# Optimization experiments

Measured on AMD Instinct MI355X. Metric: run time of the kernel, lower is better.

## Reference

```python
import jax, jax.numpy as jnp
import numpy as np

N_Q = 8        # qubits
DENC = 3       # encoding entangling layers
DVAR = 3       # variational entangling layers
SEQ = 64
BATCH = 256
D_FEAT = N_Q * (DENC + 2)   # 40, per-token feature dim
D_W = N_Q * (DVAR + 2)      # 40, per-position weight dim


def _rx(t):
    c = jnp.cos(t / 2).astype(jnp.complex64)
    s = (-1j * jnp.sin(t / 2)).astype(jnp.complex64)
    return jnp.stack([jnp.stack([c, s]), jnp.stack([s, c])])


def _ry(t):
    c = jnp.cos(t / 2)
    s = jnp.sin(t / 2)
    return jnp.stack([jnp.stack([c, -s]), jnp.stack([s, c])]).astype(jnp.complex64)


def _apply1(state, U, wire):
    # state: (2,)*N_Q complex; apply 2x2 gate on `wire`
    s = jnp.tensordot(U, state, axes=([1], [wire]))
    return jnp.moveaxis(s, 0, wire)


def _cnot(state, c, t):
    s0 = jnp.take(state, 0, axis=c)
    s1 = jnpp_flip = jnp.take(state, 1, axis=c)
    t2 = t - 1 if t > c else t
    s1 = jnp.flip(s1, axis=t2)  # X on target when control=1
    return jnp.stack([s0, s1], axis=c)


def _circuit(x, w, sign):
    # x: [D_FEAT] encoding angles, w: [D_W] variational angles
    state = jnp.zeros((2,) * N_Q, jnp.complex64).at[(0,) * N_Q].set(1.0)
    idx = 0
    for j in range(N_Q):
        state = _apply1(state, _rx(x[idx]), j)
        state = _apply1(state, _ry(x[idx + 1]), j)
        idx += 2
    for _ in range(DENC):
        for j in range(N_Q):
            state = _cnot(state, j, (j + 1) % N_Q)
        for j in range(N_Q):
            state = _apply1(state, _ry(x[idx]), j)
            idx += 1
    idx = 0
    for j in range(N_Q):
        state = _apply1(state, _rx(w[idx]), j)
        state = _apply1(state, _ry(w[idx + 1]), j)
        idx += 2
    for _ in range(DVAR):
        for j in range(N_Q):
            state = _cnot(state, j, (j + 1) % N_Q)
        for j in range(N_Q):
            state = _apply1(state, _ry(w[idx]), j)
            idx += 1
    probs = (jnp.abs(state) ** 2).astype(jnp.float32)
    return jnp.sum(probs * sign)


# observable sign tables
_Z0 = jnp.array([1.0, -1.0], jnp.float32).reshape((2,) + (1,) * (N_Q - 1))
_ZALL = jnp.array([1.0, -1.0], jnp.float32)
for _ in range(N_Q - 1):
    _ZALL = _ZALL[..., None] * jnp.array([1.0, -1.0], jnp.float32)


def _batched(sign):
    f = lambda xx, ww: _circuit(xx, ww, sign)
    f = jax.vmap(f, in_axes=(0, 0))      # over seq positions (per-position weights)
    return jax.vmap(f, in_axes=(0, None))  # over batch


_qk = _batched(_Z0)
_v = _batched(_ZALL)  # random_op fixed deterministically to Z x Z x ... x Z


def setup_inputs() -> dict:
    key = jax.random.key(0)
    k1, k2, k3, k4 = jax.random.split(key, 4)
    scale = np.float32(np.pi / 4)
    x = jax.random.normal(k1, (BATCH, SEQ, D_FEAT), jnp.float32)
    pQ = scale * (2 * jax.random.normal(k2, (SEQ, D_W), jnp.float32) - 1)
    pK = scale * (2 * jax.random.normal(k3, (SEQ, D_W), jnp.float32) - 1)
    pV = scale * (2 * jax.random.normal(k4, (SEQ, D_W), jnp.float32) - 1)
    return {"x": x, "params_Q": pQ, "params_K": pK, "params_V": pV}


def reference(x, params_Q, params_K, params_V):
    # Per-token quantum circuit sims -> scalar Q, K, V expectations
    Q = _qk(x, params_Q)   # [B, S]
    K = _qk(x, params_K)   # [B, S]
    V = _v(x, params_V)    # [B, S]  (original returns d identical copies of this)
    # Gaussian-kernel attention: alpha[b,i,m] = exp(-(Q_i - K_m)^2)
    alpha = jnp.exp(-(Q[:, :, None] - K[:, None, :]) ** 2)   # [B, S, S]
    w = alpha / jnp.sum(alpha, axis=-1, keepdims=True)
    att = jnp.einsum('bim,bm->bi', w, V)                     # [B, S]
    return x + att[:, :, None]  # broadcast over d (V copies are identical)
```

## Files before the change

### kernel.cpp

```cpp
#include <hip/hip_runtime.h>

#define SEQd 64
#define BATCHd 256
#define DF 40

typedef float f2 __attribute__((ext_vector_type(2)));
typedef __fp16 h2v __attribute__((ext_vector_type(2)));


template<int LM>
__device__ __forceinline__ float xch1(float v) {
  if constexpr (LM == 0) {
    return v;
  } else if constexpr (LM == 1 || LM == 2 || LM == 3 || LM == 7) {
    constexpr int ctrl = (LM == 1) ? 0xB1 : (LM == 2) ? 0x4E : (LM == 3) ? 0x1B
                       : 0x141;
    return __int_as_float(__builtin_amdgcn_mov_dpp(__float_as_int(v), ctrl, 0xF, 0xF, true));
  } else {
    return __int_as_float(__builtin_amdgcn_ds_swizzle(__float_as_int(v), (LM << 10) | 0x1F));
  }
}

template<int LM>
__device__ __forceinline__ f2 xch2(f2 v) {
  if constexpr (LM == 0) return v;
  f2 r; r.x = xch1<LM>(v.x); r.y = xch1<LM>(v.y); return r;
}

__device__ __forceinline__ f2 ff(f2 x, f2 y, f2 z) { return __builtin_elementwise_fma(x, y, z); }
__device__ __forceinline__ f2 cmul(f2 a, f2 b) {
  f2 r; r.x = a.x * b.x - a.y * b.y; r.y = a.x * b.y + a.y * b.x; return r;
}
__device__ __forceinline__ f2 uget(float4 f, bool bit) {
  f2 r; r.x = bit ? f.z : f.x; r.y = bit ? -f.w : f.y; return r;
}

template<int M, int SM>
__device__ __forceinline__ void ry32(f2* a, f2 cs, int lam) {
  constexpr int LM = M & 7, RM = M >> 3, SL = SM & 7, SR = SM >> 3;
  float t0;
  if constexpr (SL != 0) t0 = (__popc(lam & SL) & 1) ? cs.y : -cs.y;
  else                   t0 = -cs.y;
  const f2 cv = {cs.x, cs.x};
  const f2 tp = {t0, t0}, tn = {-t0, -t0};
#pragma unroll
  for (int k = 0; k < 32; ++k) {
    const int kp = k ^ RM;
    if (kp < k) continue;
    if (kp == k) {
      const f2 b = xch2<LM>(a[k]);
      a[k] = ff(b, (__builtin_popcount(k & SR) & 1) ? tn : tp, a[k] * cv);
    } else {
      const f2 b0 = xch2<LM>(a[kp]);
      const f2 b1 = xch2<LM>(a[k]);
      const f2 t_k  = (__builtin_popcount(k  & SR) & 1) ? tn : tp;
      const f2 t_kp = (__builtin_popcount(kp & SR) & 1) ? tn : tp;
      a[k]  = ff(b0, t_k,  a[k]  * cv);
      a[kp] = ff(b1, t_kp, a[kp] * cv);
    }
  }
}

template<int M, int SM>
__device__ __forceinline__ void su2_32(f2* a, float4 q, int lam) {
  constexpr int LM = M & 7, RM = M >> 3, SL = SM & 7, SR = SM >> 3;
  float sb, sc;
  if constexpr (SL != 0) {
    const bool p = (__popc(lam & SL) & 1) != 0;
    sb = p ? -q.y : q.y; sc = p ? -q.z : q.z;
  } else { sb = q.y; sc = q.z; }
  const f2 vqa = {q.x, q.x};
  const f2 vqw = {q.w, -q.w};
  const f2 vfc0 = {-sc, -sc}, vfb0 = {-sb, sb};
  const f2 vfc1 = { sc,  sc}, vfb1 = { sb, -sb};
#pragma unroll
  for (int k = 0; k < 32; ++k) {
    const int kp = k ^ RM;
    if (kp < k) continue;
    if (kp == k) {
      const f2 B = xch2<LM>(a[k]);
      const bool pk = (__builtin_popcount(k & SR) & 1) != 0;
      const f2 A = a[k];
      f2 r = A * vqa;
      r = ff(B, pk ? vfc1 : vfc0, r);
      r = ff(A.yx, pk ? vfb1 : vfb0, r);
      r = ff(B.yx, vqw, r);
      a[k] = r;
    } else {
      const f2 B0 = xch2<LM>(a[kp]);
      const f2 B1 = xch2<LM>(a[k]);
      const bool pk0 = (__builtin_popcount(k  & SR) & 1) != 0;
      const bool pk1 = (__builtin_popcount(kp & SR) & 1) != 0;
      const f2 A0 = a[k], A1 = a[kp];
      f2 r0 = A0 * vqa;
      r0 = ff(B0, pk0 ? vfc1 : vfc0, r0);
      r0 = ff(A0.yx, pk0 ? vfb1 : vfb0, r0);
      r0 = ff(B0.yx, vqw, r0);
      a[k] = r0;
      f2 r1 = A1 * vqa;
      r1 = ff(B1, pk1 ? vfc1 : vfc0, r1);
      r1 = ff(A1.yx, pk1 ? vfb1 : vfb0, r1);
      r1 = ff(B1.yx, vqw, r1);
      a[kp] = r1;
    }
  }
}

__device__ __forceinline__ void layers32(f2* a, const f2* __restrict__ L, int lam) {
  ry32<0xC0,0x7F>(a, L[0],  lam);
  ry32<0x60,0xC0>(a, L[1],  lam);
  ry32<0x30,0xE0>(a, L[2],  lam);
  ry32<0x18,0xF0>(a, L[3],  lam);
  ry32<0x0C,0xF8>(a, L[4],  lam);
  ry32<0x06,0xFC>(a, L[5],  lam);
  ry32<0x03,0xFE>(a, L[6],  lam);
  ry32<0xC1,0xFF>(a, L[7],  lam);
  ry32<0xA0,0xD5>(a, L[8],  lam);
  ry32<0x50,0xBF>(a, L[9],  lam);
  ry32<0x28,0x5F>(a, L[10], lam);
  ry32<0x14,0xAF>(a, L[11], lam);
  ry32<0x0A,0x57>(a, L[12], lam);
  ry32<0x05,0xAB>(a, L[13], lam);
  ry32<0xC2,0x55>(a, L[14], lam);
  ry32<0x61,0xAA>(a, L[15], lam);
  ry32<0xF0,0x4C>(a, L[16], lam);
  ry32<0x78,0x6A>(a, L[17], lam);
  ry32<0x3C,0x35>(a, L[18], lam);
  ry32<0x1E,0x9A>(a, L[19], lam);
  ry32<0x0F,0xCD>(a, L[20], lam);
  ry32<0xC7,0x66>(a, L[21], lam);
  ry32<0xA3,0x33>(a, L[22], lam);
  ry32<0x91,0x99>(a, L[23], lam);
}

__device__ __forceinline__ void initial32(f2* a, const float4* __restrict__ F, int lam) {
  su2_32<0x80,0x80>(a, F[0], lam);
  su2_32<0x40,0x40>(a, F[1], lam);
  su2_32<0x20,0x20>(a, F[2], lam);
  su2_32<0x10,0x10>(a, F[3], lam);
  su2_32<0x08,0x08>(a, F[4], lam);
  su2_32<0x04,0x04>(a, F[5], lam);
  su2_32<0x02,0x02>(a, F[6], lam);
  su2_32<0x01,0x01>(a, F[7], lam);
}

__device__ __forceinline__ void pinit32(f2* a, const float4* __restrict__ F, int lam) {
  f2 c = {1.f, 0.f};
#pragma unroll
  for (int i = 0; i < 3; ++i)
    c = cmul(c, uget(F[7 - i], ((lam >> i) & 1) != 0));
  f2 wlo[4], whi[8];
#pragma unroll
  for (int t = 0; t < 4; ++t)
    wlo[t] = cmul(uget(F[4], (t & 1) != 0), uget(F[3], ((t >> 1) & 1) != 0));
#pragma unroll
  for (int t = 0; t < 8; ++t)
    whi[t] = cmul(cmul(uget(F[2], (t & 1) != 0), uget(F[1], ((t >> 1) & 1) != 0)),
                  uget(F[0], ((t >> 2) & 1) != 0));
#pragma unroll
  for (int k = 0; k < 32; ++k)
    a[k] = cmul(cmul(c, wlo[k & 3]), whi[k >> 2]);
}

__device__ __forceinline__ uint32_t packh(f2 v) {
  h2v h = __builtin_amdgcn_cvt_pkrtz(v.x, v.y);
  return __builtin_bit_cast(uint32_t, h);
}
__device__ __forceinline__ f2 unpackh(uint32_t u) {
  h2v h = __builtin_bit_cast(h2v, u);
  f2 r; r.x = (float)h[0]; r.y = (float)h[1]; return r;
}

__device__ __forceinline__ void snap_write32(const f2* a, uint32_t* sn, int lam) {
  int tgt = 0;
  if (lam & 1) tgt ^= 0x2B;
  if (lam & 2) tgt ^= 0x56;
  if (lam & 4) tgt ^= 0xAC;
#pragma unroll
  for (int k = 0; k < 32; ++k) {
    const int rck = ((k & 1) ? 0xD9 : 0) ^ ((k & 2) ? 0x33 : 0) ^ ((k & 4) ? 0x66 : 0)
                  ^ ((k & 8) ? 0xCC : 0) ^ ((k & 16) ? 0x19 : 0);
    const int qq = tgt ^ rck;
    sn[(qq & 7) * 36 + (qq >> 3)] = packh(a[k]);
  }
}

__device__ __forceinline__ void snap_read32(f2* a, const uint32_t* sn, int lam) {
  const uint4* p = (const uint4*)(sn + lam * 36);
#pragma unroll
  for (int t = 0; t < 8; ++t) {
    const uint4 w = p[t];
    a[4*t+0] = unpackh(w.x); a[4*t+1] = unpackh(w.y);
    a[4*t+2] = unpackh(w.z); a[4*t+3] = unpackh(w.w);
  }
}

template<int SM>
__device__ __forceinline__ float expect32(const f2* a, int lam) {
  constexpr int SL = SM & 7, SR = SM >> 3;
  float s0 = 0.f, s1 = 0.f;
#pragma unroll
  for (int k = 0; k < 32; ++k) {
    const float p = a[k].x * a[k].x + a[k].y * a[k].y;
    if ((__builtin_popcount(k & SR) & 1) != 0) s1 += p; else s0 += p;
  }
  const float d = s0 - s1;
  float v;
  if constexpr (SL != 0) v = (__popc(lam & SL) & 1) ? -d : d;
  else                   v = d;
  v += xch1<1>(v); v += xch1<2>(v); v += xch1<4>(v);
  return v;
}

__global__ __launch_bounds__(256) void prep_var(
    const float* __restrict__ pQ, const float* __restrict__ pK,
    const float* __restrict__ pV, float* __restrict__ vtab)
{
  const int t = blockIdx.x * 256 + threadIdx.x;
  if (t >= SEQd * 3 * 32) return;
  const int slot = t & 31;
  const int sh = t >> 5;
  const int h = sh % 3, sp = sh / 3;
  const float* w = ((h == 0) ? pQ : (h == 1) ? pK : pV) + sp * DF;
  float* o = vtab + sh * 80;
  if (slot < 8) {
    float cx, sx, cy, sy;
    __sincosf(w[2 * slot]     * 0.5f, &sx, &cx);
    __sincosf(w[2 * slot + 1] * 0.5f, &sy, &cy);
    ((float4*)o)[slot] = make_float4(cy * cx, sy * sx, sy * cx, cy * sx);
  } else {
    float sn, cn;
    __sincosf(w[16 + (slot - 8)] * 0.5f, &sn, &cn);
    ((float2*)(o + 32))[slot - 8] = make_float2(cn, sn);
  }
}

__global__ __launch_bounds__(256, 3) void qsal_circuits(
    const float* __restrict__ x, const float* __restrict__ vtab,
    float* __restrict__ Qo, float* __restrict__ Ko, float* __restrict__ Vo)
{
  __shared__ __align__(16) float etab[32][84];
  __shared__ __align__(16) uint32_t snap[32][296];
  __shared__ __align__(16) float vtabs[240];
  const int tid = threadIdx.x;
  const int wid = tid >> 6, lane = tid & 63;
  const int lam = lane & 7;
  const int cig = (wid << 3) | (lane >> 3);
  const int s = blockIdx.x & 63;
  const int bbase = (blockIdx.x >> 6) << 5;

  for (int t = tid; t < 1280; t += 256) {
    const int cc = t / 40, idx = t - cc * 40;
    const float ang = x[((size_t)(bbase + cc) * 64 + s) * 40 + idx];
    float sn, cn; __sincosf(ang * 0.5f, &sn, &cn);
    if (idx < 16) {
      const int wire = idx >> 1, isy = idx & 1;
      etab[cc][wire * 4 + isy * 2 + 0] = cn;
      etab[cc][wire * 4 + isy * 2 + 1] = sn;
    } else {
      etab[cc][32 + (idx - 16) * 2 + 0] = cn;
      etab[cc][32 + (idx - 16) * 2 + 1] = sn;
    }
  }
  if (tid < 60) ((float4*)vtabs)[tid] = ((const float4*)(vtab + s * 240))[tid];
  __syncthreads();
  {
    const int cc = tid >> 3, wire = tid & 7;
    float4* qt = (float4*)etab[cc];
    const float4 f = qt[wire];
    qt[wire] = make_float4(f.z * f.x, f.w * f.y, f.w * f.x, f.z * f.y);
  }
  __syncthreads();

  f2 st[32];
#pragma unroll 1
  for (int ph = 0; ph < 4; ++ph) {
    const f2* L;
    if (ph == 0) {
      pinit32(st, (const float4*)etab[cig], lam);
      L = (const f2*)(etab[cig] + 32);
    } else {
      snap_read32(st, snap[cig], lam);
      const float* th = vtabs + (ph - 1) * 80;
      initial32(st, (const float4*)th, lam);
      L = (const f2*)(th + 32);
    }
    layers32(st, L, lam);
    if (ph == 0) {
      snap_write32(st, snap[cig], lam);
    } else {
      const float e = (ph == 3) ? expect32<0x88>(st, lam) : expect32<0x4C>(st, lam);
      if (lam == 0) {
        float* op = (ph == 1) ? Qo : (ph == 2) ? Ko : Vo;
        op[(bbase + cig) * 64 + s] = e;
      }
    }
    __syncthreads();
  }
}

__global__ __launch_bounds__(256) void qsal_attn(
    const float* __restrict__ x,
    const float* __restrict__ Qv,
    const float* __restrict__ Kv,
    const float* __restrict__ Vv,
    float* __restrict__ out)
{
  const int tid  = threadIdx.x;
  const int wid  = tid >> 6;
  const int lane = tid & 63;
  const int bi   = blockIdx.x * 4 + wid;
  const int b    = bi >> 6;

  const float q = Qv[bi];
  const float k = Kv[b * 64 + lane];
  const float v = Vv[b * 64 + lane];
  const float d = q - k;
  float e  = __expf(-d * d);
  float ev = e * v;
#pragma unroll
  for (int m = 1; m < 64; m <<= 1) {
    e  += __shfl_xor(e,  m, 64);
    ev += __shfl_xor(ev, m, 64);
  }
  const float att = ev / e;

  const size_t row = (size_t)bi * DF;
  if (lane < DF) out[row + lane] = x[row + lane] + att;
}

extern "C" void kernel_launch(void* const* d_in, const int* in_sizes, int n_in,
                              void* d_out, int out_size, void* d_ws, size_t ws_size,
                              hipStream_t stream) {
  const float* x  = (const float*)d_in[0];
  const float* pQ = (const float*)d_in[1];
  const float* pK = (const float*)d_in[2];
  const float* pV = (const float*)d_in[3];
  float* out = (float*)d_out;

  float* Qv   = (float*)d_ws;
  float* Kv   = Qv + BATCHd * SEQd;
  float* Vv   = Kv + BATCHd * SEQd;
  float* vtab = Vv + BATCHd * SEQd;

  prep_var<<<dim3(24), dim3(256), 0, stream>>>(pQ, pK, pV, vtab);
  qsal_circuits<<<dim3(512), dim3(256), 0, stream>>>(x, vtab, Qv, Kv, Vv);
  qsal_attn<<<dim3(BATCHd * SEQd / 4), dim3(256), 0, stream>>>(x, Qv, Kv, Vv, out);
}
```

Before: 76.90 us.

## Shrink circuit kernel to single-wave blocks and drop block barriers

The circuit kernel now launches 2048 blocks of 64 threads instead of 512 blocks of 256, so each workgroup is one wavefront. That lets every __syncthreads be removed. The variational angle table is read straight from global memory with a wave-uniform offset instead of being staged in shared memory. Shared memory per block also drops. The launch bound changes to (64,4), which may shift register allocation and occupancy, and global/scalar loads of the angle table replace LDS reads.

Result: slower. 105.4 us (+37.0%).

```diff
diff --git a/kernel.cpp b/kernel.cpp
--- a/kernel.cpp
+++ b/kernel.cpp
@@ -106,7 +106,8 @@
   }
 }
 
-__device__ __forceinline__ void layers32(f2* a, const f2* __restrict__ L, int lam) {
+template<typename CPtr>
+__device__ __forceinline__ void layers32(f2* a, CPtr L, int lam) {
   ry32<0xC0,0x7F>(a, L[0],  lam);
   ry32<0x60,0xC0>(a, L[1],  lam);
   ry32<0x30,0xE0>(a, L[2],  lam);
@@ -133,7 +134,8 @@
   ry32<0x91,0x99>(a, L[23], lam);
 }
 
-__device__ __forceinline__ void initial32(f2* a, const float4* __restrict__ F, int lam) {
+template<typename FPtr>
+__device__ __forceinline__ void initial32(f2* a, FPtr F, int lam) {
   su2_32<0x80,0x80>(a, F[0], lam);
   su2_32<0x40,0x40>(a, F[1], lam);
   su2_32<0x20,0x20>(a, F[2], lam);
@@ -144,7 +146,7 @@
   su2_32<0x01,0x01>(a, F[7], lam);
 }
 
-__device__ __forceinline__ void pinit32(f2* a, const float4* __restrict__ F, int lam) {
+__device__ __forceinline__ void pinit32(f2* a, const float4* F, int lam) {
   f2 c = {1.f, 0.f};
 #pragma unroll
   for (int i = 0; i < 3; ++i)
@@ -235,21 +237,19 @@
   }
 }
 
-__global__ __launch_bounds__(256, 3) void qsal_circuits(
+__global__ __launch_bounds__(64, 4) void qsal_circuits(
     const float* __restrict__ x, const float* __restrict__ vtab,
     float* __restrict__ Qo, float* __restrict__ Ko, float* __restrict__ Vo)
 {
-  __shared__ __align__(16) float etab[32][84];
-  __shared__ __align__(16) uint32_t snap[32][296];
-  __shared__ __align__(16) float vtabs[240];
+  __shared__ __align__(16) float etab[8][84];
+  __shared__ __align__(16) uint32_t snap[8][296];
   const int tid = threadIdx.x;
-  const int wid = tid >> 6, lane = tid & 63;
-  const int lam = lane & 7;
-  const int cig = (wid << 3) | (lane >> 3);
+  const int lam = tid & 7;
+  const int cig = tid >> 3;
   const int s = blockIdx.x & 63;
-  const int bbase = (blockIdx.x >> 6) << 5;
-
-  for (int t = tid; t < 1280; t += 256) {
+  const int bbase = (blockIdx.x >> 6) << 3;
+
+  for (int t = tid; t < 320; t += 64) {
     const int cc = t / 40, idx = t - cc * 40;
     const float ang = x[((size_t)(bbase + cc) * 64 + s) * 40 + idx];
     float sn, cn; __sincosf(ang * 0.5f, &sn, &cn);
@@ -262,40 +262,30 @@
       etab[cc][32 + (idx - 16) * 2 + 1] = sn;
     }
   }
-  if (tid < 60) ((float4*)vtabs)[tid] = ((const float4*)(vtab + s * 240))[tid];
-  __syncthreads();
   {
     const int cc = tid >> 3, wire = tid & 7;
     float4* qt = (float4*)etab[cc];
     const float4 f = qt[wire];
     qt[wire] = make_float4(f.z * f.x, f.w * f.y, f.w * f.x, f.z * f.y);
   }
-  __syncthreads();
 
   f2 st[32];
+  pinit32(st, (const float4*)etab[cig], lam);
+  layers32(st, (const f2*)(etab[cig] + 32), lam);
+  snap_write32(st, snap[cig], lam);
+
 #pragma unroll 1
-  for (int ph = 0; ph < 4; ++ph) {
-    const f2* L;
-    if (ph == 0) {
-      pinit32(st, (const float4*)etab[cig], lam);
-      L = (const f2*)(etab[cig] + 32);
-    } else {
-      snap_read32(st, snap[cig], lam);
-      const float* th = vtabs + (ph - 1) * 80;
-      initial32(st, (const float4*)th, lam);
-      L = (const f2*)(th + 32);
+  for (int h = 0; h < 3; ++h) {
+    const int voff = __builtin_amdgcn_readfirstlane(s * 240 + h * 80);
+    const float* th = vtab + voff;
+    snap_read32(st, snap[cig], lam);
+    initial32(st, (const float4*)th, lam);
+    layers32(st, (const f2*)(th + 32), lam);
+    const float e = (h == 2) ? expect32<0x88>(st, lam) : expect32<0x4C>(st, lam);
+    if (lam == 0) {
+      float* op = (h == 0) ? Qo : (h == 1) ? Ko : Vo;
+      op[(bbase + cig) * 64 + s] = e;
     }
-    layers32(st, L, lam);
-    if (ph == 0) {
-      snap_write32(st, snap[cig], lam);
-    } else {
-      const float e = (ph == 3) ? expect32<0x88>(st, lam) : expect32<0x4C>(st, lam);
-      if (lam == 0) {
-        float* op = (ph == 1) ? Qo : (ph == 2) ? Ko : Vo;
-        op[(bbase + cig) * 64 + s] = e;
-      }
-    }
-    __syncthreads();
   }
 }
 
@@ -344,6 +334,6 @@
   float* vtab = Vv + BATCHd * SEQd;
 
   prep_var<<<dim3(24), dim3(256), 0, stream>>>(pQ, pK, pV, vtab);
-  qsal_circuits<<<dim3(512), dim3(256), 0, stream>>>(x, vtab, Qv, Kv, Vv);
+  qsal_circuits<<<dim3(2048), dim3(64), 0, stream>>>(x, vtab, Qv, Kv, Vv);
   qsal_attn<<<dim3(BATCHd * SEQd / 4), dim3(256), 0, stream>>>(x, Qv, Kv, Vv, out);
 }
```

## Split circuit kernel into encoding and variational kernels via global snapshot

Applied to the files above, without the earlier changes.

Splits the monolithic circuit kernel into an encoding kernel, which writes the fp16 post-encoding state to a global workspace, and a variational kernel that runs the Q, K and V circuits in parallel wavefronts, one per head. This removes the serial phase loop and the block-wide barriers, so the three variational circuits run concurrently. In exchange it adds a global round trip of about 16 MB and one more launch. If the workspace is too small it falls back to the old monolithic kernel.

New measurement: 87.78 us. +14.2%, slower.

```diff
diff --git a/kernel.cpp b/kernel.cpp
--- a/kernel.cpp
+++ b/kernel.cpp
@@ -106,7 +106,8 @@
   }
 }
 
-__device__ __forceinline__ void layers32(f2* a, const f2* __restrict__ L, int lam) {
+template<typename CPtr>
+__device__ __forceinline__ void layers32(f2* a, CPtr L, int lam) {
   ry32<0xC0,0x7F>(a, L[0],  lam);
   ry32<0x60,0xC0>(a, L[1],  lam);
   ry32<0x30,0xE0>(a, L[2],  lam);
@@ -133,7 +134,8 @@
   ry32<0x91,0x99>(a, L[23], lam);
 }
 
-__device__ __forceinline__ void initial32(f2* a, const float4* __restrict__ F, int lam) {
+template<typename FPtr>
+__device__ __forceinline__ void initial32(f2* a, FPtr F, int lam) {
   su2_32<0x80,0x80>(a, F[0], lam);
   su2_32<0x40,0x40>(a, F[1], lam);
   su2_32<0x20,0x20>(a, F[2], lam);
@@ -144,7 +146,7 @@
   su2_32<0x01,0x01>(a, F[7], lam);
 }
 
-__device__ __forceinline__ void pinit32(f2* a, const float4* __restrict__ F, int lam) {
+__device__ __forceinline__ void pinit32(f2* a, const float4* F, int lam) {
   f2 c = {1.f, 0.f};
 #pragma unroll
   for (int i = 0; i < 3; ++i)
@@ -171,21 +173,36 @@
   f2 r; r.x = (float)h[0]; r.y = (float)h[1]; return r;
 }
 
-__device__ __forceinline__ void snap_write32(const f2* a, uint32_t* sn, int lam) {
+__device__ __forceinline__ int snap_tgt_lane(int lam) {
   int tgt = 0;
   if (lam & 1) tgt ^= 0x2B;
   if (lam & 2) tgt ^= 0x56;
   if (lam & 4) tgt ^= 0xAC;
+  return tgt;
+}
+__device__ __forceinline__ int snap_rck(int k) {
+  return ((k & 1) ? 0xD9 : 0) ^ ((k & 2) ? 0x33 : 0) ^ ((k & 4) ? 0x66 : 0)
+       ^ ((k & 8) ? 0xCC : 0) ^ ((k & 16) ? 0x19 : 0);
+}
+
+__device__ __forceinline__ void snap_write_g(const f2* a, uint32_t* sn, int lam) {
+  const int tgt = snap_tgt_lane(lam);
 #pragma unroll
   for (int k = 0; k < 32; ++k) {
-    const int rck = ((k & 1) ? 0xD9 : 0) ^ ((k & 2) ? 0x33 : 0) ^ ((k & 4) ? 0x66 : 0)
-                  ^ ((k & 8) ? 0xCC : 0) ^ ((k & 16) ? 0x19 : 0);
-    const int qq = tgt ^ rck;
+    const int qq = tgt ^ snap_rck(k);
+    sn[(qq & 7) * 32 + (qq >> 3)] = packh(a[k]);
+  }
+}
+
+__device__ __forceinline__ void snap_write_m(const f2* a, uint32_t* sn, int lam) {
+  const int tgt = snap_tgt_lane(lam);
+#pragma unroll
+  for (int k = 0; k < 32; ++k) {
+    const int qq = tgt ^ snap_rck(k);
     sn[(qq & 7) * 36 + (qq >> 3)] = packh(a[k]);
   }
 }
-
-__device__ __forceinline__ void snap_read32(f2* a, const uint32_t* sn, int lam) {
+__device__ __forceinline__ void snap_read_m(f2* a, const uint32_t* sn, int lam) {
   const uint4* p = (const uint4*)(sn + lam * 36);
 #pragma unroll
   for (int t = 0; t < 8; ++t) {
@@ -210,6 +227,29 @@
   else                   v = d;
   v += xch1<1>(v); v += xch1<2>(v); v += xch1<4>(v);
   return v;
+}
+
+__device__ __forceinline__ void fill_etab(float (*et)[84], const float* __restrict__ x,
+                                          int bbase, int s, int lane) {
+  for (int t = lane; t < 320; t += 64) {
+    const int cc = t / 40, idx = t - cc * 40;
+    const float ang = x[((size_t)(bbase + cc) * 64 + s) * 40 + idx];
+    float sn, cn; __sincosf(ang * 0.5f, &sn, &cn);
+    if (idx < 16) {
+      const int wire = idx >> 1, isy = idx & 1;
+      et[cc][wire * 4 + isy * 2 + 0] = cn;
+      et[cc][wire * 4 + isy * 2 + 1] = sn;
+    } else {
+      et[cc][32 + (idx - 16) * 2 + 0] = cn;
+      et[cc][32 + (idx - 16) * 2 + 1] = sn;
+    }
+  }
+  {
+    const int cc = lane >> 3, wire = lane & 7;
+    float4* qt = (float4*)et[cc];
+    const float4 f = qt[wire];
+    qt[wire] = make_float4(f.z * f.x, f.w * f.y, f.w * f.x, f.z * f.y);
+  }
 }
 
 __global__ __launch_bounds__(256) void prep_var(
@@ -235,7 +275,67 @@
   }
 }
 
-__global__ __launch_bounds__(256, 3) void qsal_circuits(
+__global__ __launch_bounds__(256) void qsal_enc(
+    const float* __restrict__ x, uint32_t* __restrict__ snapg)
+{
+  __shared__ __align__(16) float etab[4][8][84];
+  __shared__ __align__(16) uint32_t snap[4][8][264];
+  const int tid = threadIdx.x;
+  const int wid = tid >> 6, lane = tid & 63;
+  const int lam = lane & 7, cig = lane >> 3;
+  const int cgrp = blockIdx.x * 4 + wid;
+  const int s = cgrp & 63;
+  const int bbase = (cgrp >> 6) << 3;
+
+  fill_etab(etab[wid], x, bbase, s, lane);
+
+  f2 st[32];
+  pinit32(st, (const float4*)etab[wid][cig], lam);
+  layers32(st, (const f2*)(etab[wid][cig] + 32), lam);
+  snap_write_g(st, snap[wid][cig], lam);
+
+  uint32_t* gb = snapg + ((size_t)cgrp * 8 + cig) * 256;
+#pragma unroll
+  for (int r = 0; r < 8; ++r) {
+    const int u4 = lam + 8 * r;
+    const uint4 v = *(const uint4*)&snap[wid][cig][u4 * 4];
+    ((uint4*)gb)[u4] = v;
+  }
+}
+
+__global__ __launch_bounds__(192) void qsal_var(
+    const uint32_t* __restrict__ snapg, const float* __restrict__ vtab,
+    float* __restrict__ Qo, float* __restrict__ Ko, float* __restrict__ Vo)
+{
+  __shared__ __align__(16) float ltab[3][80];
+  const int tid = threadIdx.x;
+  const int h = tid / 64, lane = tid & 63;
+  const int lam = lane & 7, cig = lane >> 3;
+  const int cgrp = blockIdx.x;
+  const int s = cgrp & 63;
+  const int bbase = (cgrp >> 6) << 3;
+
+  if (lane < 20)
+    ((float4*)ltab[h])[lane] = ((const float4*)(vtab + s * 240 + h * 80))[lane];
+
+  f2 st[32];
+  const uint4* sp = (const uint4*)(snapg + (((size_t)cgrp * 8 + cig) * 256 + lam * 32));
+#pragma unroll
+  for (int t = 0; t < 8; ++t) {
+    const uint4 w = sp[t];
+    st[4*t+0] = unpackh(w.x); st[4*t+1] = unpackh(w.y);
+    st[4*t+2] = unpackh(w.z); st[4*t+3] = unpackh(w.w);
+  }
+  initial32(st, (const float4*)ltab[h], lam);
+  layers32(st, (const f2*)(ltab[h] + 32), lam);
+  const float e = (h == 2) ? expect32<0x88>(st, lam) : expect32<0x4C>(st, lam);
+  if (lam == 0) {
+    float* op = (h == 0) ? Qo : (h == 1) ? Ko : Vo;
+    op[(bbase + cig) * 64 + s] = e;
+  }
+}
+
+__global__ __launch_bounds__(256, 3) void qsal_mono(
     const float* __restrict__ x, const float* __restrict__ vtab,
     float* __restrict__ Qo, float* __restrict__ Ko, float* __restrict__ Vo)
 {
@@ -280,14 +380,14 @@
       pinit32(st, (const float4*)etab[cig], lam);
       L = (const f2*)(etab[cig] + 32);
     } else {
-      snap_read32(st, snap[cig], lam);
+      snap_read_m(st, snap[cig], lam);
       const float* th = vtabs + (ph - 1) * 80;
       initial32(st, (const float4*)th, lam);
       L = (const f2*)(th + 32);
     }
     layers32(st, L, lam);
     if (ph == 0) {
-      snap_write32(st, snap[cig], lam);
+      snap_write_m(st, snap[cig], lam);
     } else {
       const float e = (ph == 3) ? expect32<0x88>(st, lam) : expect32<0x4C>(st, lam);
       if (lam == 0) {
@@ -338,12 +438,21 @@
   const float* pV = (const float*)d_in[3];
   float* out = (float*)d_out;
 
+  const int NC = BATCHd * SEQd;
   float* Qv   = (float*)d_ws;
-  float* Kv   = Qv + BATCHd * SEQd;
-  float* Vv   = Kv + BATCHd * SEQd;
-  float* vtab = Vv + BATCHd * SEQd;
+  float* Kv   = Qv + NC;
+  float* Vv   = Kv + NC;
+  float* vtab = Vv + NC;
+  uint32_t* snapg = (uint32_t*)(vtab + SEQd * 3 * 80);
+
+  const size_t need = (size_t)(3 * NC + SEQd * 3 * 80) * 4 + (size_t)NC * 256 * 4;
 
   prep_var<<<dim3(24), dim3(256), 0, stream>>>(pQ, pK, pV, vtab);
-  qsal_circuits<<<dim3(512), dim3(256), 0, stream>>>(x, vtab, Qv, Kv, Vv);
-  qsal_attn<<<dim3(BATCHd * SEQd / 4), dim3(256), 0, stream>>>(x, Qv, Kv, Vv, out);
-}
+  if (ws_size >= need) {
+    qsal_enc<<<dim3(512), dim3(256), 0, stream>>>(x, snapg);
+    qsal_var<<<dim3(2048), dim3(192), 0, stream>>>(snapg, vtab, Qv, Kv, Vv);
+  } else {
+    qsal_mono<<<dim3(512), dim3(256), 0, stream>>>(x, vtab, Qv, Kv, Vv);
+  }
+  qsal_attn<<<dim3(NC / 4), dim3(256), 0, stream>>>(x, Qv, Kv, Vv, out);
+}
```

## Split statevector into real/imag planes and use inline packed FP32 FMA asm

Applied to the files above, without the earlier changes.

Each thread's 32 complex amplitudes move from interleaved (re,im) pairs to separate real and imaginary arrays, each packing two adjacent basis states. The gate kernels are rewritten as compile-time recursive templates that emit v_pk_mul_f32/v_pk_fma_f32 through inline asm, using op_sel and neg modifiers for sign flips and element swaps. The aim is to remove the swizzles and per-element negations the compiler inserted for the interleaved complex form, so every gate update runs on packed math. Inline asm hides these instructions from the scheduler, and the snapshot read/write and expectation code must reshuffle between the two layouts.

New measurement: 77.90 us. About the same (+1.3%).

```diff
diff --git a/kernel.cpp b/kernel.cpp
--- a/kernel.cpp
+++ b/kernel.cpp
@@ -7,6 +7,8 @@
 typedef float f2 __attribute__((ext_vector_type(2)));
 typedef __fp16 h2v __attribute__((ext_vector_type(2)));
 
+
+__device__ __forceinline__ f2 mkf2(float a, float b) { f2 r; r.x = a; r.y = b; return r; }
 
 template<int LM>
 __device__ __forceinline__ float xch1(float v) {
@@ -27,7 +29,28 @@
   f2 r; r.x = xch1<LM>(v.x); r.y = xch1<LM>(v.y); return r;
 }
 
-__device__ __forceinline__ f2 ff(f2 x, f2 y, f2 z) { return __builtin_elementwise_fma(x, y, z); }
+__device__ __forceinline__ f2 pkmul(f2 a, f2 b) {
+  f2 d;
+  asm("v_pk_mul_f32 %0, %1, %2" : "=v"(d) : "v"(a), "v"(b));
+  return d;
+}
+template<bool NEGB, bool SWAPA>
+__device__ __forceinline__ f2 pkfma(f2 a, f2 b, f2 c) {
+  f2 d;
+  if constexpr (!NEGB && !SWAPA)
+    asm("v_pk_fma_f32 %0, %1, %2, %3" : "=v"(d) : "v"(a), "v"(b), "v"(c));
+  else if constexpr (NEGB && !SWAPA)
+    asm("v_pk_fma_f32 %0, %1, %2, %3 neg_lo:[0,1,0] neg_hi:[0,1,0]"
+        : "=v"(d) : "v"(a), "v"(b), "v"(c));
+  else if constexpr (!NEGB && SWAPA)
+    asm("v_pk_fma_f32 %0, %1, %2, %3 op_sel:[1,0,0] op_sel_hi:[0,1,1]"
+        : "=v"(d) : "v"(a), "v"(b), "v"(c));
+  else
+    asm("v_pk_fma_f32 %0, %1, %2, %3 op_sel:[1,0,0] op_sel_hi:[0,1,1] neg_lo:[0,1,0] neg_hi:[0,1,0]"
+        : "=v"(d) : "v"(a), "v"(b), "v"(c));
+  return d;
+}
+
 __device__ __forceinline__ f2 cmul(f2 a, f2 b) {
   f2 r; r.x = a.x * b.x - a.y * b.y; r.y = a.x * b.y + a.y * b.x; return r;
 }
@@ -35,117 +58,155 @@
   f2 r; r.x = bit ? f.z : f.x; r.y = bit ? -f.w : f.y; return r;
 }
 
+template<int M, int SM, int J>
+__device__ __forceinline__ void ry_rec(f2* rr, f2* ii, f2 CC, f2 TV) {
+  if constexpr (J < 16) {
+    constexpr int LM = M & 7, RM = M >> 3;
+    constexpr int RJ = RM >> 1;
+    constexpr bool R0 = (RM & 1) != 0;
+    constexpr int JP = J ^ RJ;
+    if constexpr (JP >= J) {
+      constexpr int SRj = (SM >> 3) >> 1;
+      constexpr bool PJ = (__builtin_popcount(J & SRj) & 1) != 0;
+      if constexpr (JP == J) {
+        const f2 br = xch2<LM>(rr[J]);
+        const f2 bi = xch2<LM>(ii[J]);
+        rr[J] = pkfma<PJ, R0>(br, TV, pkmul(rr[J], CC));
+        ii[J] = pkfma<PJ, R0>(bi, TV, pkmul(ii[J], CC));
+      } else {
+        constexpr bool PJP = (__builtin_popcount(JP & SRj) & 1) != 0;
+        const f2 br0 = xch2<LM>(rr[JP]);
+        const f2 bi0 = xch2<LM>(ii[JP]);
+        const f2 br1 = xch2<LM>(rr[J]);
+        const f2 bi1 = xch2<LM>(ii[J]);
+        rr[J]  = pkfma<PJ,  R0>(br0, TV, pkmul(rr[J],  CC));
+        ii[J]  = pkfma<PJ,  R0>(bi0, TV, pkmul(ii[J],  CC));
+        rr[JP] = pkfma<PJP, R0>(br1, TV, pkmul(rr[JP], CC));
+        ii[JP] = pkfma<PJP, R0>(bi1, TV, pkmul(ii[JP], CC));
+      }
+    }
+    ry_rec<M, SM, J + 1>(rr, ii, CC, TV);
+  }
+}
+
 template<int M, int SM>
-__device__ __forceinline__ void ry32(f2* a, f2 cs, int lam) {
-  constexpr int LM = M & 7, RM = M >> 3, SL = SM & 7, SR = SM >> 3;
+__device__ __forceinline__ void ry32s(f2* rr, f2* ii, f2 cs, int lam) {
+  constexpr int SL = SM & 7;
+  constexpr bool S0v = ((SM >> 3) & 1) != 0;
   float t0;
   if constexpr (SL != 0) t0 = (__popc(lam & SL) & 1) ? cs.y : -cs.y;
   else                   t0 = -cs.y;
-  const f2 cv = {cs.x, cs.x};
-  const f2 tp = {t0, t0}, tn = {-t0, -t0};
-#pragma unroll
-  for (int k = 0; k < 32; ++k) {
-    const int kp = k ^ RM;
-    if (kp < k) continue;
-    if (kp == k) {
-      const f2 b = xch2<LM>(a[k]);
-      a[k] = ff(b, (__builtin_popcount(k & SR) & 1) ? tn : tp, a[k] * cv);
-    } else {
-      const f2 b0 = xch2<LM>(a[kp]);
-      const f2 b1 = xch2<LM>(a[k]);
-      const f2 t_k  = (__builtin_popcount(k  & SR) & 1) ? tn : tp;
-      const f2 t_kp = (__builtin_popcount(kp & SR) & 1) ? tn : tp;
-      a[k]  = ff(b0, t_k,  a[k]  * cv);
-      a[kp] = ff(b1, t_kp, a[kp] * cv);
+  const f2 CC = mkf2(cs.x, cs.x);
+  const f2 TV = mkf2(t0, S0v ? -t0 : t0);
+  ry_rec<M, SM, 0>(rr, ii, CC, TV);
+}
+
+template<int M, int SM, int J>
+__device__ __forceinline__ void su2_rec(f2* rr, f2* ii, f2 QX, f2 QW, f2 SC, f2 SB) {
+  if constexpr (J < 16) {
+    constexpr int LM = M & 7, RM = M >> 3;
+    constexpr int RJ = RM >> 1;
+    constexpr bool R0 = (RM & 1) != 0;
+    constexpr int JP = J ^ RJ;
+    if constexpr (JP >= J) {
+      constexpr int SRj = (SM >> 3) >> 1;
+      constexpr bool PJ = (__builtin_popcount(J & SRj) & 1) != 0;
+      if constexpr (JP == J) {
+        const f2 br = xch2<LM>(rr[J]);
+        const f2 bi = xch2<LM>(ii[J]);
+        f2 t = pkmul(rr[J], QX);
+        t = pkfma<!PJ, R0>(br, SC, t);
+        t = pkfma<!PJ, false>(ii[J], SB, t);
+        t = pkfma<false, R0>(bi, QW, t);
+        f2 u = pkmul(ii[J], QX);
+        u = pkfma<!PJ, R0>(bi, SC, u);
+        u = pkfma<PJ, false>(rr[J], SB, u);
+        u = pkfma<true, R0>(br, QW, u);
+        rr[J] = t; ii[J] = u;
+      } else {
+        constexpr bool PJP = (__builtin_popcount(JP & SRj) & 1) != 0;
+        const f2 br0 = xch2<LM>(rr[JP]);
+        const f2 bi0 = xch2<LM>(ii[JP]);
+        const f2 br1 = xch2<LM>(rr[J]);
+        const f2 bi1 = xch2<LM>(ii[J]);
+        f2 t0v = pkmul(rr[J], QX);
+        t0v = pkfma<!PJ, R0>(br0, SC, t0v);
+        t0v = pkfma<!PJ, false>(ii[J], SB, t0v);
+        t0v = pkfma<false, R0>(bi0, QW, t0v);
+        f2 u0v = pkmul(ii[J], QX);
+        u0v = pkfma<!PJ, R0>(bi0, SC, u0v);
+        u0v = pkfma<PJ, false>(rr[J], SB, u0v);
+        u0v = pkfma<true, R0>(br0, QW, u0v);
+        f2 t1v = pkmul(rr[JP], QX);
+        t1v = pkfma<!PJP, R0>(br1, SC, t1v);
+        t1v = pkfma<!PJP, false>(ii[JP], SB, t1v);
+        t1v = pkfma<false, R0>(bi1, QW, t1v);
+        f2 u1v = pkmul(ii[JP], QX);
+        u1v = pkfma<!PJP, R0>(bi1, SC, u1v);
+        u1v = pkfma<PJP, false>(rr[JP], SB, u1v);
+        u1v = pkfma<true, R0>(br1, QW, u1v);
+        rr[J] = t0v; ii[J] = u0v; rr[JP] = t1v; ii[JP] = u1v;
+      }
     }
+    su2_rec<M, SM, J + 1>(rr, ii, QX, QW, SC, SB);
   }
 }
 
 template<int M, int SM>
-__device__ __forceinline__ void su2_32(f2* a, float4 q, int lam) {
-  constexpr int LM = M & 7, RM = M >> 3, SL = SM & 7, SR = SM >> 3;
+__device__ __forceinline__ void su2g(f2* rr, f2* ii, float4 q, int lam) {
+  constexpr int SL = SM & 7;
+  constexpr bool S0v = ((SM >> 3) & 1) != 0;
   float sb, sc;
   if constexpr (SL != 0) {
     const bool p = (__popc(lam & SL) & 1) != 0;
     sb = p ? -q.y : q.y; sc = p ? -q.z : q.z;
   } else { sb = q.y; sc = q.z; }
-  const f2 vqa = {q.x, q.x};
-  const f2 vqw = {q.w, -q.w};
-  const f2 vfc0 = {-sc, -sc}, vfb0 = {-sb, sb};
-  const f2 vfc1 = { sc,  sc}, vfb1 = { sb, -sb};
-#pragma unroll
-  for (int k = 0; k < 32; ++k) {
-    const int kp = k ^ RM;
-    if (kp < k) continue;
-    if (kp == k) {
-      const f2 B = xch2<LM>(a[k]);
-      const bool pk = (__builtin_popcount(k & SR) & 1) != 0;
-      const f2 A = a[k];
-      f2 r = A * vqa;
-      r = ff(B, pk ? vfc1 : vfc0, r);
-      r = ff(A.yx, pk ? vfb1 : vfb0, r);
-      r = ff(B.yx, vqw, r);
-      a[k] = r;
-    } else {
-      const f2 B0 = xch2<LM>(a[kp]);
-      const f2 B1 = xch2<LM>(a[k]);
-      const bool pk0 = (__builtin_popcount(k  & SR) & 1) != 0;
-      const bool pk1 = (__builtin_popcount(kp & SR) & 1) != 0;
-      const f2 A0 = a[k], A1 = a[kp];
-      f2 r0 = A0 * vqa;
-      r0 = ff(B0, pk0 ? vfc1 : vfc0, r0);
-      r0 = ff(A0.yx, pk0 ? vfb1 : vfb0, r0);
-      r0 = ff(B0.yx, vqw, r0);
-      a[k] = r0;
-      f2 r1 = A1 * vqa;
-      r1 = ff(B1, pk1 ? vfc1 : vfc0, r1);
-      r1 = ff(A1.yx, pk1 ? vfb1 : vfb0, r1);
-      r1 = ff(B1.yx, vqw, r1);
-      a[kp] = r1;
-    }
-  }
-}
-
-__device__ __forceinline__ void layers32(f2* a, const f2* __restrict__ L, int lam) {
-  ry32<0xC0,0x7F>(a, L[0],  lam);
-  ry32<0x60,0xC0>(a, L[1],  lam);
-  ry32<0x30,0xE0>(a, L[2],  lam);
-  ry32<0x18,0xF0>(a, L[3],  lam);
-  ry32<0x0C,0xF8>(a, L[4],  lam);
-  ry32<0x06,0xFC>(a, L[5],  lam);
-  ry32<0x03,0xFE>(a, L[6],  lam);
-  ry32<0xC1,0xFF>(a, L[7],  lam);
-  ry32<0xA0,0xD5>(a, L[8],  lam);
-  ry32<0x50,0xBF>(a, L[9],  lam);
-  ry32<0x28,0x5F>(a, L[10], lam);
-  ry32<0x14,0xAF>(a, L[11], lam);
-  ry32<0x0A,0x57>(a, L[12], lam);
-  ry32<0x05,0xAB>(a, L[13], lam);
-  ry32<0xC2,0x55>(a, L[14], lam);
-  ry32<0x61,0xAA>(a, L[15], lam);
-  ry32<0xF0,0x4C>(a, L[16], lam);
-  ry32<0x78,0x6A>(a, L[17], lam);
-  ry32<0x3C,0x35>(a, L[18], lam);
-  ry32<0x1E,0x9A>(a, L[19], lam);
-  ry32<0x0F,0xCD>(a, L[20], lam);
-  ry32<0xC7,0x66>(a, L[21], lam);
-  ry32<0xA3,0x33>(a, L[22], lam);
-  ry32<0x91,0x99>(a, L[23], lam);
-}
-
-__device__ __forceinline__ void initial32(f2* a, const float4* __restrict__ F, int lam) {
-  su2_32<0x80,0x80>(a, F[0], lam);
-  su2_32<0x40,0x40>(a, F[1], lam);
-  su2_32<0x20,0x20>(a, F[2], lam);
-  su2_32<0x10,0x10>(a, F[3], lam);
-  su2_32<0x08,0x08>(a, F[4], lam);
-  su2_32<0x04,0x04>(a, F[5], lam);
-  su2_32<0x02,0x02>(a, F[6], lam);
-  su2_32<0x01,0x01>(a, F[7], lam);
-}
-
-__device__ __forceinline__ void pinit32(f2* a, const float4* __restrict__ F, int lam) {
-  f2 c = {1.f, 0.f};
+  const f2 QX = mkf2(q.x, q.x), QW = mkf2(q.w, q.w);
+  const f2 SCv = mkf2(sc, S0v ? -sc : sc);
+  const f2 SBv = mkf2(sb, S0v ? -sb : sb);
+  su2_rec<M, SM, 0>(rr, ii, QX, QW, SCv, SBv);
+}
+
+__device__ __forceinline__ void layers32s(f2* rr, f2* ii, const f2* L, int lam) {
+  ry32s<0xC0,0x7F>(rr, ii, L[0],  lam);
+  ry32s<0x60,0xC0>(rr, ii, L[1],  lam);
+  ry32s<0x30,0xE0>(rr, ii, L[2],  lam);
+  ry32s<0x18,0xF0>(rr, ii, L[3],  lam);
+  ry32s<0x0C,0xF8>(rr, ii, L[4],  lam);
+  ry32s<0x06,0xFC>(rr, ii, L[5],  lam);
+  ry32s<0x03,0xFE>(rr, ii, L[6],  lam);
+  ry32s<0xC1,0xFF>(rr, ii, L[7],  lam);
+  ry32s<0xA0,0xD5>(rr, ii, L[8],  lam);
+  ry32s<0x50,0xBF>(rr, ii, L[9],  lam);
+  ry32s<0x28,0x5F>(rr, ii, L[10], lam);
+  ry32s<0x14,0xAF>(rr, ii, L[11], lam);
+  ry32s<0x0A,0x57>(rr, ii, L[12], lam);
+  ry32s<0x05,0xAB>(rr, ii, L[13], lam);
+  ry32s<0xC2,0x55>(rr, ii, L[14], lam);
+  ry32s<0x61,0xAA>(rr, ii, L[15], lam);
+  ry32s<0xF0,0x4C>(rr, ii, L[16], lam);
+  ry32s<0x78,0x6A>(rr, ii, L[17], lam);
+  ry32s<0x3C,0x35>(rr, ii, L[18], lam);
+  ry32s<0x1E,0x9A>(rr, ii, L[19], lam);
+  ry32s<0x0F,0xCD>(rr, ii, L[20], lam);
+  ry32s<0xC7,0x66>(rr, ii, L[21], lam);
+  ry32s<0xA3,0x33>(rr, ii, L[22], lam);
+  ry32s<0x91,0x99>(rr, ii, L[23], lam);
+}
+
+__device__ __forceinline__ void initial32s(f2* rr, f2* ii, const float4* F, int lam) {
+  su2g<0x80,0x80>(rr, ii, F[0], lam);
+  su2g<0x40,0x40>(rr, ii, F[1], lam);
+  su2g<0x20,0x20>(rr, ii, F[2], lam);
+  su2g<0x10,0x10>(rr, ii, F[3], lam);
+  su2g<0x08,0x08>(rr, ii, F[4], lam);
+  su2g<0x04,0x04>(rr, ii, F[5], lam);
+  su2g<0x02,0x02>(rr, ii, F[6], lam);
+  su2g<0x01,0x01>(rr, ii, F[7], lam);
+}
+
+__device__ __forceinline__ void pinit32s(f2* rr, f2* ii, const float4* F, int lam) {
+  f2 c = mkf2(1.f, 0.f);
 #pragma unroll
   for (int i = 0; i < 3; ++i)
     c = cmul(c, uget(F[7 - i], ((lam >> i) & 1) != 0));
@@ -158,12 +219,15 @@
     whi[t] = cmul(cmul(uget(F[2], (t & 1) != 0), uget(F[1], ((t >> 1) & 1) != 0)),
                   uget(F[0], ((t >> 2) & 1) != 0));
 #pragma unroll
-  for (int k = 0; k < 32; ++k)
-    a[k] = cmul(cmul(c, wlo[k & 3]), whi[k >> 2]);
-}
-
-__device__ __forceinline__ uint32_t packh(f2 v) {
-  h2v h = __builtin_amdgcn_cvt_pkrtz(v.x, v.y);
+  for (int k = 0; k < 32; ++k) {
+    const f2 a = cmul(cmul(c, wlo[k & 3]), whi[k >> 2]);
+    rr[k >> 1][k & 1] = a.x;
+    ii[k >> 1][k & 1] = a.y;
+  }
+}
+
+__device__ __forceinline__ uint32_t packh(float a, float b) {
+  h2v h = __builtin_amdgcn_cvt_pkrtz(a, b);
   return __builtin_bit_cast(uint32_t, h);
 }
 __device__ __forceinline__ f2 unpackh(uint32_t u) {
@@ -171,40 +235,53 @@
   f2 r; r.x = (float)h[0]; r.y = (float)h[1]; return r;
 }
 
-__device__ __forceinline__ void snap_write32(const f2* a, uint32_t* sn, int lam) {
+__device__ __forceinline__ int snap_tgt_lane(int lam) {
   int tgt = 0;
   if (lam & 1) tgt ^= 0x2B;
   if (lam & 2) tgt ^= 0x56;
   if (lam & 4) tgt ^= 0xAC;
+  return tgt;
+}
+__device__ __forceinline__ int snap_rck(int k) {
+  return ((k & 1) ? 0xD9 : 0) ^ ((k & 2) ? 0x33 : 0) ^ ((k & 4) ? 0x66 : 0)
+       ^ ((k & 8) ? 0xCC : 0) ^ ((k & 16) ? 0x19 : 0);
+}
+
+__device__ __forceinline__ void snap_write_s(const f2* rr, const f2* ii, uint32_t* sn, int lam) {
+  const int tgt = snap_tgt_lane(lam);
 #pragma unroll
   for (int k = 0; k < 32; ++k) {
-    const int rck = ((k & 1) ? 0xD9 : 0) ^ ((k & 2) ? 0x33 : 0) ^ ((k & 4) ? 0x66 : 0)
-                  ^ ((k & 8) ? 0xCC : 0) ^ ((k & 16) ? 0x19 : 0);
-    const int qq = tgt ^ rck;
-    sn[(qq & 7) * 36 + (qq >> 3)] = packh(a[k]);
-  }
-}
-
-__device__ __forceinline__ void snap_read32(f2* a, const uint32_t* sn, int lam) {
+    const int qq = tgt ^ snap_rck(k);
+    sn[(qq & 7) * 36 + (qq >> 3)] = packh(rr[k >> 1][k & 1], ii[k >> 1][k & 1]);
+  }
+}
+
+__device__ __forceinline__ void snap_read_s(f2* rr, f2* ii, const uint32_t* sn, int lam) {
   const uint4* p = (const uint4*)(sn + lam * 36);
 #pragma unroll
   for (int t = 0; t < 8; ++t) {
     const uint4 w = p[t];
-    a[4*t+0] = unpackh(w.x); a[4*t+1] = unpackh(w.y);
-    a[4*t+2] = unpackh(w.z); a[4*t+3] = unpackh(w.w);
+    const f2 a0 = unpackh(w.x), a1 = unpackh(w.y), a2 = unpackh(w.z), a3 = unpackh(w.w);
+    rr[2 * t]     = mkf2(a0.x, a1.x);  ii[2 * t]     = mkf2(a0.y, a1.y);
+    rr[2 * t + 1] = mkf2(a2.x, a3.x);  ii[2 * t + 1] = mkf2(a2.y, a3.y);
   }
 }
 
 template<int SM>
-__device__ __forceinline__ float expect32(const f2* a, int lam) {
+__device__ __forceinline__ float expect32s(const f2* rr, const f2* ii, int lam) {
   constexpr int SL = SM & 7, SR = SM >> 3;
-  float s0 = 0.f, s1 = 0.f;
-#pragma unroll
-  for (int k = 0; k < 32; ++k) {
-    const float p = a[k].x * a[k].x + a[k].y * a[k].y;
-    if ((__builtin_popcount(k & SR) & 1) != 0) s1 += p; else s0 += p;
-  }
-  const float d = s0 - s1;
+  constexpr int SRj = SR >> 1;
+  constexpr bool S0v = (SR & 1) != 0;
+  float d = 0.f;
+#pragma unroll
+  for (int j = 0; j < 16; ++j) {
+    const f2 pp = pkfma<false, false>(ii[j], ii[j], pkmul(rr[j], rr[j]));
+    float contrib;
+    if constexpr (S0v) contrib = pp.x - pp.y;
+    else               contrib = pp.x + pp.y;
+    const bool pj = (__builtin_popcount(j & SRj) & 1) != 0;
+    d += pj ? -contrib : contrib;
+  }
   float v;
   if constexpr (SL != 0) v = (__popc(lam & SL) & 1) ? -d : d;
   else                   v = d;
@@ -235,7 +312,7 @@
   }
 }
 
-__global__ __launch_bounds__(256, 3) void qsal_circuits(
+__global__ __launch_bounds__(256, 3) void qsal_mono(
     const float* __restrict__ x, const float* __restrict__ vtab,
     float* __restrict__ Qo, float* __restrict__ Ko, float* __restrict__ Vo)
 {
@@ -272,24 +349,25 @@
   }
   __syncthreads();
 
-  f2 st[32];
+  f2 rr[16], ii[16];
 #pragma unroll 1
   for (int ph = 0; ph < 4; ++ph) {
     const f2* L;
     if (ph == 0) {
-      pinit32(st, (const float4*)etab[cig], lam);
+      pinit32s(rr, ii, (const float4*)etab[cig], lam);
       L = (const f2*)(etab[cig] + 32);
     } else {
-      snap_read32(st, snap[cig], lam);
+      snap_read_s(rr, ii, snap[cig], lam);
       const float* th = vtabs + (ph - 1) * 80;
-      initial32(st, (const float4*)th, lam);
+      initial32s(rr, ii, (const float4*)th, lam);
       L = (const f2*)(th + 32);
     }
-    layers32(st, L, lam);
+    layers32s(rr, ii, L, lam);
     if (ph == 0) {
-      snap_write32(st, snap[cig], lam);
+      snap_write_s(rr, ii, snap[cig], lam);
     } else {
-      const float e = (ph == 3) ? expect32<0x88>(st, lam) : expect32<0x4C>(st, lam);
+      const float e = (ph == 3) ? expect32s<0x88>(rr, ii, lam)
+                                : expect32s<0x4C>(rr, ii, lam);
       if (lam == 0) {
         float* op = (ph == 1) ? Qo : (ph == 2) ? Ko : Vo;
         op[(bbase + cig) * 64 + s] = e;
@@ -338,12 +416,13 @@
   const float* pV = (const float*)d_in[3];
   float* out = (float*)d_out;
 
+  const int NC = BATCHd * SEQd;
   float* Qv   = (float*)d_ws;
-  float* Kv   = Qv + BATCHd * SEQd;
-  float* Vv   = Kv + BATCHd * SEQd;
-  float* vtab = Vv + BATCHd * SEQd;
+  float* Kv   = Qv + NC;
+  float* Vv   = Kv + NC;
+  float* vtab = Vv + NC;
 
   prep_var<<<dim3(24), dim3(256), 0, stream>>>(pQ, pK, pV, vtab);
-  qsal_circuits<<<dim3(512), dim3(256), 0, stream>>>(x, vtab, Qv, Kv, Vv);
-  qsal_attn<<<dim3(BATCHd * SEQd / 4), dim3(256), 0, stream>>>(x, Qv, Kv, Vv, out);
-}
+  qsal_mono<<<dim3(512), dim3(256), 0, stream>>>(x, vtab, Qv, Kv, Vv);
+  qsal_attn<<<dim3(NC / 4), dim3(256), 0, stream>>>(x, Qv, Kv, Vv, out);
+}
```
